# Kernel optimization log

Measured on AMD Instinct MI355X. Metric: run time of the kernel, lower is better.

## Reference

```python
import jax, jax.numpy as jnp
import numpy as np

N = 100_000   # nodes
E = 1_600_000 # edges
D = 64        # in = hidden = out channels
EPS = 1e-8


def setup_inputs() -> dict:
    key = jax.random.key(0)
    ks = jax.random.split(key, 6)
    s = 1.0 / np.sqrt(D)
    return {
        "x": jax.random.normal(ks[0], (N, D), jnp.float32),
        "edge_index": jax.random.randint(ks[1], (2, E), 0, N, dtype=jnp.int32),
        "W0": jax.random.normal(ks[2], (D, D), jnp.float32) * s,
        "b0": jnp.zeros((D,), jnp.float32),
        "Wm": jax.random.normal(ks[3], (D, D), jnp.float32) * s,
        "bm": jnp.zeros((D,), jnp.float32),
        "W1": jax.random.normal(ks[4], (D, D), jnp.float32) * s,
        "b1": jnp.zeros((D,), jnp.float32),
    }


def _proj_normalize(y):
    # projective (hyperbolic) renormalization onto the unit sphere in R^D
    return y / (jnp.linalg.norm(y, axis=-1, keepdims=True) + EPS)


def _hyp_linear(x, W, b):
    return _proj_normalize(x @ W + b)


def _hinner(u, v):
    # UHG (hyperbolic) bilinear form: <u,v> = u_1..d-1 . v_1..d-1 - u_d * v_d
    return jnp.sum(u[..., :-1] * v[..., :-1], axis=-1) - u[..., -1] * v[..., -1]


def _cross_ratio(x):
    a, b, c, d = x[0], x[1], x[2], x[3]
    return (_hinner(a, c) * _hinner(b, d)) / (_hinner(a, d) * _hinner(b, c) + EPS)


def _maybe_restore_cr(x, cr_init):
    # restore_cross_ratio: rescale x so the 4-point cross-ratio matches cr_init,
    # applied only when the torch guard conditions hold (finite, non-degenerate).
    cr_cur = _cross_ratio(x[:4])
    ratio = cr_init / (cr_cur + EPS)
    cond = ((~jnp.isnan(cr_cur)) & (~jnp.isnan(cr_init))
            & (jnp.abs(cr_cur) > EPS) & (jnp.abs(cr_init) > EPS)
            & (ratio > EPS))
    scale = jnp.where(cond, jnp.sqrt(jnp.abs(ratio)), 1.0)
    x_r = x * scale
    ok = jnp.all(jnp.isfinite(x_r))
    return jnp.where(cond & ok, x_r, x)


def _message_passing(x, src, dst, Wm, bm):
    # gather -> mean-aggregate(scatter) -> hyperbolic linear, preserving cross-ratio
    cr0 = _cross_ratio(x[:4])
    msgs = x[src]                                                  # [E, D] gather
    summed = jax.ops.segment_sum(msgs, dst, num_segments=N)        # [N, D] scatter-add
    cnt = jax.ops.segment_sum(jnp.ones((E,), x.dtype), dst, num_segments=N)
    agg = summed / jnp.maximum(cnt, 1.0)[:, None]                  # mean aggregation
    h = _proj_normalize(agg @ Wm + bm)
    return _maybe_restore_cr(h, cr0)


def reference(x, edge_index, W0, b0, Wm, bm, W1, b1):
    src, dst = edge_index[0], edge_index[1]
    cr_init = _cross_ratio(x[:4])          # N > 3 so has_cr is always True
    h = _hyp_linear(x, W0, b0)             # layers[0]
    # num_layers = 2 -> single message-passing round (i = 1)
    h = _message_passing(h, src, dst, Wm, bm)
    h = _hyp_linear(h, W1, b1)             # layers[1]
    h = jax.nn.relu(h)                      # act
    h = _maybe_restore_cr(h, cr_init)
    return h
```

## Files before the change

kernel.cpp:

```cpp
#include <hip/hip_runtime.h>
#include <math.h>

#define NNODES 100000
#define NEDGES 1600000
#define DD 64
#define EPS 1e-8f

#define NBUCK 1024
#define BW 98
#define BIN_BLOCKS 256
#define BIN_CHUNK ((NEDGES + BIN_BLOCKS - 1) / BIN_BLOCKS)
#define BIN_CAP 12
#define CAPB 1792
#define SORT_CAP 4096
#define NTILES (NNODES / 16)
#define CAP4 512
#define TSTR 68

typedef unsigned short us8 __attribute__((ext_vector_type(8)));
typedef short short8 __attribute__((ext_vector_type(8)));
typedef float f32x4 __attribute__((ext_vector_type(4)));

__device__ __forceinline__ float wave_sum(float v) {
    #pragma unroll
    for (int off = 32; off; off >>= 1) v += __shfl_xor(v, off, 64);
    return v;
}

__device__ __forceinline__ float hinner(float u, float v, float sgn) {
    return wave_sum(sgn * u * v);
}

__device__ __forceinline__ float cross_ratio(float r0, float r1, float r2, float r3, float sgn) {
    float A = hinner(r0, r2, sgn);
    float B = hinner(r1, r3, sgn);
    float C = hinner(r0, r3, sgn);
    float Dv = hinner(r1, r2, sgn);
    return (A * B) / (C * Dv + EPS);
}

__device__ __forceinline__ float restore_scale(float cr_i, float cr_c) {
    float ratio = cr_i / (cr_c + EPS);
    bool cond = (!__builtin_isnan(cr_c)) && (!__builtin_isnan(cr_i)) &&
                (fabsf(cr_c) > EPS) && (fabsf(cr_i) > EPS) && (ratio > EPS);
    float s = 1.0f;
    if (cond) {
        s = sqrtf(fabsf(ratio));
        if (!__builtin_isfinite(s)) s = 1.0f;
    }
    return s;
}

__device__ __forceinline__ unsigned short f2bf(float f) {
    unsigned u = __float_as_uint(f);
    unsigned r = (u + 0x7fffu + ((u >> 16) & 1u)) >> 16;
    return (unsigned short)r;
}

__device__ __forceinline__ float bf2f(unsigned short b) {
    return __uint_as_float(((unsigned)b) << 16);
}

__device__ __forceinline__ float bcast(float v, int lane) {
    return __int_as_float(__builtin_amdgcn_readlane(__float_as_int(v), lane));
}

__device__ __forceinline__ void load_bfrags(const float* __restrict__ W, int lane,
                                            short8 bhi[4][2], short8 blo[4][2]) {
    int c = lane & 15, q = lane >> 4;
    #pragma unroll
    for (int t = 0; t < 4; t++)
        #pragma unroll
        for (int h = 0; h < 2; h++) {
            short8 hi8, lo8;
            #pragma unroll
            for (int j = 0; j < 8; j++) {
                float w = W[(h * 32 + q * 8 + j) * DD + t * 16 + c];
                unsigned short hb = f2bf(w);
                float r = w - bf2f(hb);
                hi8[j] = (short)hb;
                lo8[j] = (short)f2bf(r);
            }
            bhi[t][h] = hi8;
            blo[t][h] = lo8;
        }
}

__device__ __forceinline__ void build_a8(const float av[8], short8& hi, short8& lo) {
    short8 h8, l8;
    #pragma unroll
    for (int j = 0; j < 8; j++) {
        unsigned short hb = f2bf(av[j]);
        float r = av[j] - bf2f(hb);
        h8[j] = (short)hb;
        l8[j] = (short)f2bf(r);
    }
    hi = h8;
    lo = l8;
}

__device__ __forceinline__ void build_a(const float* p, short8& hi, short8& lo) {
    float4 f0 = *(const float4*)p;
    float4 f1 = *(const float4*)(p + 4);
    float av[8] = {f0.x, f0.y, f0.z, f0.w, f1.x, f1.y, f1.z, f1.w};
    build_a8(av, hi, lo);
}

__device__ __forceinline__ void store_split(unsigned short* __restrict__ aggh,
                                            int node, int q, const float* s, float inv) {
    short8 hi8, lo8;
    #pragma unroll
    for (int i = 0; i < 8; i++) {
        float v = s[i] * inv;
        unsigned short hb = f2bf(v);
        hi8[i] = (short)hb;
        lo8[i] = (short)f2bf(v - bf2f(hb));
    }
    unsigned short* p = aggh + (size_t)node * 128 + q * 16;
    *(short8*)p = hi8;
    *(short8*)(p + 8) = lo8;
}

#define MFMA3R(cacc, ahi, alo, BH, BL, t, h)                                     \
    cacc = __builtin_amdgcn_mfma_f32_16x16x32_bf16(ahi, BH[t][h], cacc, 0, 0, 0); \
    cacc = __builtin_amdgcn_mfma_f32_16x16x32_bf16(alo, BH[t][h], cacc, 0, 0, 0); \
    cacc = __builtin_amdgcn_mfma_f32_16x16x32_bf16(ahi, BL[t][h], cacc, 0, 0, 0);

__device__ __forceinline__ void l0_tiles(const float* __restrict__ x,
                                         const float* __restrict__ W0,
                                         const float* __restrict__ b0,
                                         unsigned short* __restrict__ h0b,
                                         int lane, int wid, int nw, int tlo, int thi) {
    int c = lane & 15, q = lane >> 4;
    short8 bhi[4][2], blo[4][2];
    load_bfrags(W0, lane, bhi, blo);
    float badd[4];
    #pragma unroll
    for (int t = 0; t < 4; t++) badd[t] = b0[t * 16 + c];
    for (int tile = tlo + wid; tile < thi; tile += nw) {
        int R = tile * 16;
        f32x4 cc[4] = {{0, 0, 0, 0}, {0, 0, 0, 0}, {0, 0, 0, 0}, {0, 0, 0, 0}};
        #pragma unroll
        for (int hh = 0; hh < 2; hh++) {
            short8 ahi, alo;
            build_a(x + ((size_t)(R + c) << 6) + hh * 32 + q * 8, ahi, alo);
            #pragma unroll
            for (int t = 0; t < 4; t++) { MFMA3R(cc[t], ahi, alo, bhi, blo, t, hh); }
        }
        float ss[4];
        #pragma unroll
        for (int r = 0; r < 4; r++) {
            #pragma unroll
            for (int t = 0; t < 4; t++) cc[t][r] += badd[t];
            ss[r] = cc[0][r] * cc[0][r] + cc[1][r] * cc[1][r] +
                    cc[2][r] * cc[2][r] + cc[3][r] * cc[3][r];
        }
        #pragma unroll
        for (int off = 1; off <= 8; off <<= 1) {
            #pragma unroll
            for (int r = 0; r < 4; r++) ss[r] += __shfl_xor(ss[r], off, 64);
        }
        #pragma unroll
        for (int r = 0; r < 4; r++) {
            float sc = 1.0f / (sqrtf(ss[r]) + EPS);
            int row = R + q * 4 + r;
            #pragma unroll
            for (int t = 0; t < 4; t++)
                h0b[(size_t)row * DD + t * 16 + c] = f2bf(cc[t][r] * sc);
        }
    }
}

__global__ __launch_bounds__(256, 3) void k_binGemm(const float* __restrict__ x,
                                                    const float* __restrict__ W0,
                                                    const float* __restrict__ b0,
                                                    unsigned short* __restrict__ h0b,
                                                    const int* __restrict__ ei,
                                                    int* __restrict__ cursor,
                                                    unsigned* __restrict__ colpack,
                                                    int* __restrict__ cnt4,
                                                    int* __restrict__ list4) {
    __shared__ unsigned stag[NBUCK * BIN_CAP];
    __shared__ int lcnt[NBUCK];
    int t = threadIdx.x;
    if (blockIdx.x < BIN_BLOCKS) {
        for (int i = t; i < NBUCK; i += 256) lcnt[i] = 0;
        __syncthreads();
        int lo = blockIdx.x * BIN_CHUNK;
        int hi = lo + BIN_CHUNK; if (hi > NEDGES) hi = NEDGES;
        for (int e = lo + t; e < hi; e += 256) {
            int d = ei[NEDGES + e];
            int s = ei[e];
            if ((unsigned)d < 4u) {
                int p = atomicAdd(&cnt4[d], 1);
                if (p < CAP4) list4[d * CAP4 + p] = s;
            }
            unsigned b = (unsigned)d / BW;
            unsigned dl = (unsigned)d - b * BW;
            unsigned pk = ((unsigned)s << 8) | dl;
            int slot = atomicAdd(&lcnt[b], 1);
            if (slot < BIN_CAP) {
                stag[b * BIN_CAP + slot] = pk;
            } else {
                colpack[b * CAPB + atomicAdd(&cursor[b], 1)] = pk;
            }
        }
        __syncthreads();
        for (int b = t; b < NBUCK; b += 256) {
            int cnt = lcnt[b];
            if (cnt > BIN_CAP) cnt = BIN_CAP;
            if (cnt > 0) {
                int base = b * CAPB + atomicAdd(&cursor[b], cnt);
                for (int i = 0; i < cnt; i++)
                    colpack[base + i] = stag[b * BIN_CAP + i];
            }
        }
        return;
    }
    int bid = blockIdx.x - BIN_BLOCKS;
    int wid = (bid * 256 + t) >> 6;
    l0_tiles(x, W0, b0, h0b, t & 63, wid, 4096, 0, NTILES);
}

__global__ __launch_bounds__(512, 4) void k_sortAggH(const unsigned* __restrict__ colpack,
                                                     const int* __restrict__ cursor,
                                                     const unsigned short* __restrict__ h0b,
                                                     unsigned short* __restrict__ aggh,
                                                     const float* __restrict__ x,
                                                     const float* __restrict__ W0,
                                                     const float* __restrict__ b0,
                                                     const int* __restrict__ cnt4,
                                                     const int* __restrict__ list4,
                                                     const float* __restrict__ Wm,
                                                     const float* __restrict__ bm,
                                                     const float* __restrict__ W1,
                                                     const float* __restrict__ b1,
                                                     float* __restrict__ scal) {
    __shared__ int lcol[SORT_CAP];
    __shared__ int cnt[BW];
    __shared__ int pre[BW];
    int t = threadIdx.x;
    if (blockIdx.x == 0) {
        float* hs  = (float*)lcol;
        float* h2s = hs + 4 * DD;
        float* frs = h2s + 4 * DD;
        int lane = t & 63;
        int w = t >> 6;
        float sgn = (lane == 63) ? -1.0f : 1.0f;
        float s1 = 1.0f;
        float cr_init = 0.0f;
        if (w < 4) {
            float w0[DD];
            #pragma unroll
            for (int k = 0; k < DD; k++) w0[k] = W0[k * DD + lane];
            float b0v = b0[lane];
            auto h0row = [&](int r) -> float {
                float xv = x[(size_t)r * DD + lane];
                float acc = b0v;
                #pragma unroll
                for (int k = 0; k < DD; k++)
                    acc = fmaf(bcast(xv, k), w0[k], acc);
                float n = sqrtf(wave_sum(acc * acc));
                return acc / (n + EPS);
            };
            hs[w * DD + lane] = h0row(w);
            int full = cnt4[w];
            int cl = full; if (cl > CAP4) cl = CAP4;
            float sum = 0.0f;
            for (int i = 0; i < cl; i++) sum += h0row(list4[w * CAP4 + i]);
            float av = sum / fmaxf((float)full, 1.0f);
            float acc = bm[lane];
            #pragma unroll
            for (int k = 0; k < DD; k++)
                acc = fmaf(bcast(av, k), Wm[k * DD + lane], acc);
            float n = sqrtf(wave_sum(acc * acc));
            h2s[w * DD + lane] = acc / (n + EPS);
        }
        __syncthreads();
        if (w < 4) {
            cr_init = cross_ratio(x[lane], x[DD + lane], x[2 * DD + lane], x[3 * DD + lane], sgn);
            float cr0 = cross_ratio(hs[lane], hs[DD + lane], hs[2 * DD + lane], hs[3 * DD + lane], sgn);
            float cr_cur = cross_ratio(h2s[lane], h2s[DD + lane], h2s[2 * DD + lane], h2s[3 * DD + lane], sgn);
            s1 = restore_scale(cr0, cr_cur);
            float hv = h2s[w * DD + lane] * s1;
            float acc2 = b1[lane];
            #pragma unroll
            for (int k = 0; k < DD; k++)
                acc2 = fmaf(bcast(hv, k), W1[k * DD + lane], acc2);
            float n = sqrtf(wave_sum(acc2 * acc2));
            frs[w * DD + lane] = fmaxf(acc2 / (n + EPS), 0.0f);
        }
        __syncthreads();
        if (w == 0) {
            float cr2 = cross_ratio(frs[lane], frs[DD + lane], frs[2 * DD + lane], frs[3 * DD + lane], sgn);
            float s2 = restore_scale(cr_init, cr2);
            if (lane == 0) { scal[0] = s1; scal[1] = s2; }
        }
        return;
    }
    int b = blockIdx.x - 1;
    int nlo = b * BW; if (nlo > NNODES) nlo = NNODES;
    int nhi = nlo + BW; if (nhi > NNODES) nhi = NNODES;
    int nodes = nhi - nlo;
    int base = b * CAPB;
    int n = cursor[b];
    if (n > CAPB) n = CAPB;
    for (int i = t; i < BW; i += 512) cnt[i] = 0;
    __syncthreads();
    for (int i = t; i < n; i += 512)
        atomicAdd(&cnt[colpack[base + i] & 255u], 1);
    __syncthreads();
    if (t < 64) {
        int v0 = cnt[t];
        int inc0 = v0;
        #pragma unroll
        for (int off = 1; off < 64; off <<= 1) {
            int u = __shfl_up(inc0, off, 64);
            if (t >= off) inc0 += u;
        }
        int tot0 = __builtin_amdgcn_readlane(inc0, 63);
        int ex0 = inc0 - v0;
        int i1 = 64 + t;
        int v1 = (i1 < BW) ? cnt[i1] : 0;
        int inc1 = v1;
        #pragma unroll
        for (int off = 1; off < 64; off <<= 1) {
            int u = __shfl_up(inc1, off, 64);
            if (t >= off) inc1 += u;
        }
        int ex1 = inc1 - v1 + tot0;
        pre[t] = ex0;
        cnt[t] = ex0;
        if (i1 < BW) { pre[i1] = ex1; cnt[i1] = ex1; }
    }
    __syncthreads();
    for (int i = t; i < n; i += 512) {
        unsigned pk = colpack[base + i];
        int pos = atomicAdd(&cnt[pk & 255u], 1);
        lcol[pos] = (int)(pk >> 8);
    }
    __syncthreads();
    int wv = t >> 6, lane = t & 63;
    int q = lane & 7, g = lane >> 3;
    for (int dA = wv; dA < nodes; dA += 32) {
        int dB = dA + 8, dC = dA + 16, dD = dA + 24;
        bool hB = dB < nodes, hC = dC < nodes, hD = dD < nodes;
        int stA = pre[dA], enA = cnt[dA];
        int stB = hB ? pre[dB] : 0, enB = hB ? cnt[dB] : 0;
        int stC = hC ? pre[dC] : 0, enC = hC ? cnt[dC] : 0;
        int stD = hD ? pre[dD] : 0, enD = hD ? cnt[dD] : 0;
        int ngA = (enA - stA + 7) >> 3, ngB = (enB - stB + 7) >> 3;
        int ngC = (enC - stC + 7) >> 3, ngD = (enD - stD + 7) >> 3;
        int ng = ngA > ngB ? ngA : ngB;
        if (ngC > ng) ng = ngC;
        if (ngD > ng) ng = ngD;
        float sA[8] = {0, 0, 0, 0, 0, 0, 0, 0};
        float sB[8] = {0, 0, 0, 0, 0, 0, 0, 0};
        float sC[8] = {0, 0, 0, 0, 0, 0, 0, 0};
        float sD[8] = {0, 0, 0, 0, 0, 0, 0, 0};
        for (int k = 0; k < ng; k++) {
            int eA = stA + k * 8 + g;
            int eB = stB + k * 8 + g;
            int eC = stC + k * 8 + g;
            int eD = stD + k * 8 + g;
            bool fA = eA < enA, fB = eB < enB, fC = eC < enC, fD = eD < enD;
            int iA = lcol[fA ? eA : 0];
            int iB = lcol[fB ? eB : 0];
            int iC = lcol[fC ? eC : 0];
            int iD = lcol[fD ? eD : 0];
            us8 uA = *(const us8*)(h0b + (size_t)iA * DD + q * 8);
            us8 uB = *(const us8*)(h0b + (size_t)iB * DD + q * 8);
            us8 uC = *(const us8*)(h0b + (size_t)iC * DD + q * 8);
            us8 uD = *(const us8*)(h0b + (size_t)iD * DD + q * 8);
            float mA = fA ? 1.0f : 0.0f;
            float mB = fB ? 1.0f : 0.0f;
            float mC = fC ? 1.0f : 0.0f;
            float mD = fD ? 1.0f : 0.0f;
            #pragma unroll
            for (int i = 0; i < 8; i++) {
                sA[i] = fmaf(mA, bf2f(uA[i]), sA[i]);
                sB[i] = fmaf(mB, bf2f(uB[i]), sB[i]);
                sC[i] = fmaf(mC, bf2f(uC[i]), sC[i]);
                sD[i] = fmaf(mD, bf2f(uD[i]), sD[i]);
            }
        }
        #pragma unroll
        for (int i = 0; i < 8; i++) {
            sA[i] += __shfl_xor(sA[i], 8, 64);
            sA[i] += __shfl_xor(sA[i], 16, 64);
            sA[i] += __shfl_xor(sA[i], 32, 64);
            sB[i] += __shfl_xor(sB[i], 8, 64);
            sB[i] += __shfl_xor(sB[i], 16, 64);
            sB[i] += __shfl_xor(sB[i], 32, 64);
            sC[i] += __shfl_xor(sC[i], 8, 64);
            sC[i] += __shfl_xor(sC[i], 16, 64);
            sC[i] += __shfl_xor(sC[i], 32, 64);
            sD[i] += __shfl_xor(sD[i], 8, 64);
            sD[i] += __shfl_xor(sD[i], 16, 64);
            sD[i] += __shfl_xor(sD[i], 32, 64);
        }
        if (g == 0) {
            store_split(aggh, nlo + dA, q, sA, 1.0f / fmaxf((float)(enA - stA), 1.0f));
            if (hB) store_split(aggh, nlo + dB, q, sB, 1.0f / fmaxf((float)(enB - stB), 1.0f));
            if (hC) store_split(aggh, nlo + dC, q, sC, 1.0f / fmaxf((float)(enC - stC), 1.0f));
            if (hD) store_split(aggh, nlo + dD, q, sD, 1.0f / fmaxf((float)(enD - stD), 1.0f));
        }
    }
}

__global__ __launch_bounds__(256, 2) void k_gemm2(unsigned short* __restrict__ dataH,
                                                  float* __restrict__ outp,
                                                  const float* __restrict__ Wm,
                                                  const float* __restrict__ bm,
                                                  const float* __restrict__ W1,
                                                  const float* __restrict__ b1,
                                                  const float* __restrict__ scal) {
    __shared__ float tsm[4][16 * TSTR];
    int tid = threadIdx.x;
    int wv = tid >> 6, lane = tid & 63;
    int c = lane & 15, q = lane >> 4;
    short8 bhiM[4][2], bloM[4][2], bhi1[4][2], blo1[4][2];
    load_bfrags(Wm, lane, bhiM, bloM);
    load_bfrags(W1, lane, bhi1, blo1);
    float bmv[4], b1v[4];
    #pragma unroll
    for (int t = 0; t < 4; t++) { bmv[t] = bm[t * 16 + c]; b1v[t] = b1[t * 16 + c]; }
    float s1 = scal[0], s2 = scal[1];
    int wid = (blockIdx.x * 256 + tid) >> 6;
    int nw = (gridDim.x * 256) >> 6;
    for (int tile = wid; tile < NTILES; tile += nw) {
        int R = tile * 16;
        f32x4 cc[4] = {{0, 0, 0, 0}, {0, 0, 0, 0}, {0, 0, 0, 0}, {0, 0, 0, 0}};
        #pragma unroll
        for (int hh = 0; hh < 2; hh++) {
            const unsigned short* p = dataH + (size_t)(R + c) * 128 + (hh * 4 + q) * 16;
            short8 ahi = *(const short8*)p;
            short8 alo = *(const short8*)(p + 8);
            #pragma unroll
            for (int t = 0; t < 4; t++) { MFMA3R(cc[t], ahi, alo, bhiM, bloM, t, hh); }
        }
        float ss[4];
        #pragma unroll
        for (int r = 0; r < 4; r++) {
            #pragma unroll
            for (int t = 0; t < 4; t++) cc[t][r] += bmv[t];
            ss[r] = cc[0][r] * cc[0][r] + cc[1][r] * cc[1][r] +
                    cc[2][r] * cc[2][r] + cc[3][r] * cc[3][r];
        }
        #pragma unroll
        for (int off = 1; off <= 8; off <<= 1) {
            #pragma unroll
            for (int r = 0; r < 4; r++) ss[r] += __shfl_xor(ss[r], off, 64);
        }
        #pragma unroll
        for (int r = 0; r < 4; r++) {
            float sc = s1 / (sqrtf(ss[r]) + EPS);
            #pragma unroll
            for (int t = 0; t < 4; t++)
                tsm[wv][(q * 4 + r) * TSTR + t * 16 + c] = cc[t][r] * sc;
        }
        f32x4 c2[4] = {{0, 0, 0, 0}, {0, 0, 0, 0}, {0, 0, 0, 0}, {0, 0, 0, 0}};
        #pragma unroll
        for (int hh = 0; hh < 2; hh++) {
            const float* p = &tsm[wv][c * TSTR + hh * 32 + q * 8];
            float av[8];
            #pragma unroll
            for (int j = 0; j < 8; j++) av[j] = p[j];
            short8 ahi, alo;
            build_a8(av, ahi, alo);
            #pragma unroll
            for (int t = 0; t < 4; t++) { MFMA3R(c2[t], ahi, alo, bhi1, blo1, t, hh); }
        }
        #pragma unroll
        for (int r = 0; r < 4; r++) {
            #pragma unroll
            for (int t = 0; t < 4; t++) c2[t][r] += b1v[t];
            ss[r] = c2[0][r] * c2[0][r] + c2[1][r] * c2[1][r] +
                    c2[2][r] * c2[2][r] + c2[3][r] * c2[3][r];
        }
        #pragma unroll
        for (int off = 1; off <= 8; off <<= 1) {
            #pragma unroll
            for (int r = 0; r < 4; r++) ss[r] += __shfl_xor(ss[r], off, 64);
        }
        #pragma unroll
        for (int r = 0; r < 4; r++) {
            float sc = 1.0f / (sqrtf(ss[r]) + EPS);
            int row = R + q * 4 + r;
            #pragma unroll
            for (int t = 0; t < 4; t++)
                outp[(size_t)row * DD + t * 16 + c] = fmaxf(c2[t][r] * sc, 0.0f) * s2;
        }
    }
}

extern "C" void kernel_launch(void* const* d_in, const int* in_sizes, int n_in,
                              void* d_out, int out_size, void* d_ws, size_t ws_size,
                              hipStream_t stream) {
    const float* x  = (const float*)d_in[0];
    const int*   ei = (const int*)d_in[1];
    const float* W0 = (const float*)d_in[2];
    const float* b0 = (const float*)d_in[3];
    const float* Wm = (const float*)d_in[4];
    const float* bm = (const float*)d_in[5];
    const float* W1 = (const float*)d_in[6];
    const float* b1 = (const float*)d_in[7];
    float* out = (float*)d_out;
    unsigned short* outH = (unsigned short*)d_out;

    unsigned short* h0b = (unsigned short*)d_ws;
    unsigned* colpack = (unsigned*)(h0b + (size_t)NNODES * DD);
    int* cursor = (int*)(colpack + (size_t)NBUCK * CAPB);
    int* cnt4   = cursor + NBUCK;
    int* list4  = cnt4 + 4;
    float* scal = (float*)(list4 + 4 * CAP4);

    (void)hipMemsetAsync(cursor, 0, (NBUCK + 4) * sizeof(int), stream);

    k_binGemm <<<BIN_BLOCKS + 1024, 256, 0, stream>>>(x, W0, b0, h0b, ei, cursor,
                                                      colpack, cnt4, list4);
    k_sortAggH<<<NBUCK, 512, 0, stream>>>(colpack, cursor, h0b, outH,
                                          x, W0, b0, cnt4, list4, Wm, bm, W1, b1, scal);
    k_gemm2   <<<512, 256, 0, stream>>>(outH, out, Wm, bm, W1, b1, scal);
}
```

Before: 185.2 us.

## Fuse Wm hyperbolic linear into aggregation kernel via LDS staging

The aggregation kernel now stages each bucket's mean-aggregated rows as split bf16 hi/lo in shared memory, then runs the Wm GEMM plus row normalization in-block and writes the normalized result to global. The final kernel only does the W1 GEMM, folding the s1 restore scale algebraically into the accumulator (s1*acc + b1), and launches with more blocks. This removes the intermediate shared-memory round trip and the second GEMM from the last kernel, at the cost of more LDS per aggregation block (a staging buffer), a zeroing pass, and scalar 2-byte global stores that may coalesce poorly.

```diff
diff --git a/kernel.cpp b/kernel.cpp
--- a/kernel.cpp
+++ b/kernel.cpp
@@ -12,10 +12,9 @@
 #define BIN_CHUNK ((NEDGES + BIN_BLOCKS - 1) / BIN_BLOCKS)
 #define BIN_CAP 12
 #define CAPB 1792
-#define SORT_CAP 4096
 #define NTILES (NNODES / 16)
 #define CAP4 512
-#define TSTR 68
+#define SROW 136
 
 typedef unsigned short us8 __attribute__((ext_vector_type(8)));
 typedef short short8 __attribute__((ext_vector_type(8)));
@@ -104,21 +103,6 @@
     float4 f1 = *(const float4*)(p + 4);
     float av[8] = {f0.x, f0.y, f0.z, f0.w, f1.x, f1.y, f1.z, f1.w};
     build_a8(av, hi, lo);
-}
-
-__device__ __forceinline__ void store_split(unsigned short* __restrict__ aggh,
-                                            int node, int q, const float* s, float inv) {
-    short8 hi8, lo8;
-    #pragma unroll
-    for (int i = 0; i < 8; i++) {
-        float v = s[i] * inv;
-        unsigned short hb = f2bf(v);
-        hi8[i] = (short)hb;
-        lo8[i] = (short)f2bf(v - bf2f(hb));
-    }
-    unsigned short* p = aggh + (size_t)node * 128 + q * 16;
-    *(short8*)p = hi8;
-    *(short8*)(p + 8) = lo8;
 }
 
 #define MFMA3R(cacc, ahi, alo, BH, BL, t, h)                                     \
@@ -236,12 +220,13 @@
                                                      const float* __restrict__ W1,
                                                      const float* __restrict__ b1,
                                                      float* __restrict__ scal) {
-    __shared__ int lcol[SORT_CAP];
+    __shared__ int lcol[CAPB];
     __shared__ int cnt[BW];
     __shared__ int pre[BW];
+    __shared__ unsigned short stage[112 * SROW];
     int t = threadIdx.x;
     if (blockIdx.x == 0) {
-        float* hs  = (float*)lcol;
+        float* hs  = (float*)stage;
         float* h2s = hs + 4 * DD;
         float* frs = h2s + 4 * DD;
         int lane = t & 63;
@@ -306,6 +291,10 @@
     int n = cursor[b];
     if (n > CAPB) n = CAPB;
     for (int i = t; i < BW; i += 512) cnt[i] = 0;
+    {
+        int* sz = (int*)stage;
+        for (int i = t; i < (112 * SROW) / 2; i += 512) sz[i] = 0;
+    }
     __syncthreads();
     for (int i = t; i < n; i += 512)
         atomicAdd(&cnt[colpack[base + i] & 255u], 1);
@@ -400,31 +389,96 @@
             sD[i] += __shfl_xor(sD[i], 32, 64);
         }
         if (g == 0) {
-            store_split(aggh, nlo + dA, q, sA, 1.0f / fmaxf((float)(enA - stA), 1.0f));
-            if (hB) store_split(aggh, nlo + dB, q, sB, 1.0f / fmaxf((float)(enB - stB), 1.0f));
-            if (hC) store_split(aggh, nlo + dC, q, sC, 1.0f / fmaxf((float)(enC - stC), 1.0f));
-            if (hD) store_split(aggh, nlo + dD, q, sD, 1.0f / fmaxf((float)(enD - stD), 1.0f));
-        }
-    }
-}
-
-__global__ __launch_bounds__(256, 2) void k_gemm2(unsigned short* __restrict__ dataH,
+            float invs[4] = {1.0f / fmaxf((float)(enA - stA), 1.0f),
+                             1.0f / fmaxf((float)(enB - stB), 1.0f),
+                             1.0f / fmaxf((float)(enC - stC), 1.0f),
+                             1.0f / fmaxf((float)(enD - stD), 1.0f)};
+            const float* sp[4] = {sA, sB, sC, sD};
+            int dls[4] = {dA, dB, dC, dD};
+            bool hv[4] = {true, hB, hC, hD};
+            #pragma unroll
+            for (int u = 0; u < 4; u++) {
+                if (!hv[u]) continue;
+                short8 hi8, lo8;
+                #pragma unroll
+                for (int i = 0; i < 8; i++) {
+                    float v = sp[u][i] * invs[u];
+                    unsigned short hb = f2bf(v);
+                    hi8[i] = (short)hb;
+                    lo8[i] = (short)f2bf(v - bf2f(hb));
+                }
+                unsigned short* p = stage + dls[u] * SROW + q * 16;
+                *(short8*)p = hi8;
+                *(short8*)(p + 8) = lo8;
+            }
+        }
+    }
+    __syncthreads();
+    int ntile = (nodes + 15) >> 4;
+    if (wv < ntile) {
+        int c16 = lane & 15, q4 = lane >> 4;
+        short8 bhiM[4][2], bloM[4][2];
+        load_bfrags(Wm, lane, bhiM, bloM);
+        float bmv[4];
+        #pragma unroll
+        for (int tt = 0; tt < 4; tt++) bmv[tt] = bm[tt * 16 + c16];
+        int Rl = wv * 16;
+        f32x4 cm[4] = {{0, 0, 0, 0}, {0, 0, 0, 0}, {0, 0, 0, 0}, {0, 0, 0, 0}};
+        #pragma unroll
+        for (int hh = 0; hh < 2; hh++) {
+            const unsigned short* p = stage + (Rl + c16) * SROW + (hh * 4 + q4) * 16;
+            short8 ahi = *(const short8*)p;
+            short8 alo = *(const short8*)(p + 8);
+            #pragma unroll
+            for (int tt = 0; tt < 4; tt++) { MFMA3R(cm[tt], ahi, alo, bhiM, bloM, tt, hh); }
+        }
+        float ss[4];
+        #pragma unroll
+        for (int r = 0; r < 4; r++) {
+            #pragma unroll
+            for (int tt = 0; tt < 4; tt++) cm[tt][r] += bmv[tt];
+            ss[r] = cm[0][r] * cm[0][r] + cm[1][r] * cm[1][r] +
+                    cm[2][r] * cm[2][r] + cm[3][r] * cm[3][r];
+        }
+        #pragma unroll
+        for (int off = 1; off <= 8; off <<= 1) {
+            #pragma unroll
+            for (int r = 0; r < 4; r++) ss[r] += __shfl_xor(ss[r], off, 64);
+        }
+        #pragma unroll
+        for (int r = 0; r < 4; r++) {
+            float sc = 1.0f / (sqrtf(ss[r]) + EPS);
+            int row = Rl + q4 * 4 + r;
+            if (row < nodes) {
+                size_t gb = (size_t)(nlo + row) * 128;
+                int ch = (c16 >> 3);
+                int el = c16 & 7;
+                #pragma unroll
+                for (int tt = 0; tt < 4; tt++) {
+                    float v = cm[tt][r] * sc;
+                    unsigned short hb = f2bf(v);
+                    unsigned short lb = f2bf(v - bf2f(hb));
+                    aggh[gb + (2 * tt + ch) * 16 + el] = hb;
+                    aggh[gb + (2 * tt + ch) * 16 + 8 + el] = lb;
+                }
+            }
+        }
+    }
+}
+
+__global__ __launch_bounds__(256, 4) void k_gemm1(const unsigned short* __restrict__ dataH,
                                                   float* __restrict__ outp,
-                                                  const float* __restrict__ Wm,
-                                                  const float* __restrict__ bm,
                                                   const float* __restrict__ W1,
                                                   const float* __restrict__ b1,
                                                   const float* __restrict__ scal) {
-    __shared__ float tsm[4][16 * TSTR];
     int tid = threadIdx.x;
-    int wv = tid >> 6, lane = tid & 63;
+    int lane = tid & 63;
     int c = lane & 15, q = lane >> 4;
-    short8 bhiM[4][2], bloM[4][2], bhi1[4][2], blo1[4][2];
-    load_bfrags(Wm, lane, bhiM, bloM);
-    load_bfrags(W1, lane, bhi1, blo1);
-    float bmv[4], b1v[4];
+    short8 bhi[4][2], blo[4][2];
+    load_bfrags(W1, lane, bhi, blo);
+    float badd[4];
     #pragma unroll
-    for (int t = 0; t < 4; t++) { bmv[t] = bm[t * 16 + c]; b1v[t] = b1[t * 16 + c]; }
+    for (int t = 0; t < 4; t++) badd[t] = b1[t * 16 + c];
     float s1 = scal[0], s2 = scal[1];
     int wid = (blockIdx.x * 256 + tid) >> 6;
     int nw = (gridDim.x * 256) >> 6;
@@ -437,46 +491,15 @@
             short8 ahi = *(const short8*)p;
             short8 alo = *(const short8*)(p + 8);
             #pragma unroll
-            for (int t = 0; t < 4; t++) { MFMA3R(cc[t], ahi, alo, bhiM, bloM, t, hh); }
+            for (int t = 0; t < 4; t++) { MFMA3R(cc[t], ahi, alo, bhi, blo, t, hh); }
         }
         float ss[4];
         #pragma unroll
         for (int r = 0; r < 4; r++) {
             #pragma unroll
-            for (int t = 0; t < 4; t++) cc[t][r] += bmv[t];
+            for (int t = 0; t < 4; t++) cc[t][r] = s1 * cc[t][r] + badd[t];
             ss[r] = cc[0][r] * cc[0][r] + cc[1][r] * cc[1][r] +
                     cc[2][r] * cc[2][r] + cc[3][r] * cc[3][r];
-        }
-        #pragma unroll
-        for (int off = 1; off <= 8; off <<= 1) {
-            #pragma unroll
-            for (int r = 0; r < 4; r++) ss[r] += __shfl_xor(ss[r], off, 64);
-        }
-        #pragma unroll
-        for (int r = 0; r < 4; r++) {
-            float sc = s1 / (sqrtf(ss[r]) + EPS);
-            #pragma unroll
-            for (int t = 0; t < 4; t++)
-                tsm[wv][(q * 4 + r) * TSTR + t * 16 + c] = cc[t][r] * sc;
-        }
-        f32x4 c2[4] = {{0, 0, 0, 0}, {0, 0, 0, 0}, {0, 0, 0, 0}, {0, 0, 0, 0}};
-        #pragma unroll
-        for (int hh = 0; hh < 2; hh++) {
-            const float* p = &tsm[wv][c * TSTR + hh * 32 + q * 8];
-            float av[8];
-            #pragma unroll
-            for (int j = 0; j < 8; j++) av[j] = p[j];
-            short8 ahi, alo;
-            build_a8(av, ahi, alo);
-            #pragma unroll
-            for (int t = 0; t < 4; t++) { MFMA3R(c2[t], ahi, alo, bhi1, blo1, t, hh); }
-        }
-        #pragma unroll
-        for (int r = 0; r < 4; r++) {
-            #pragma unroll
-            for (int t = 0; t < 4; t++) c2[t][r] += b1v[t];
-            ss[r] = c2[0][r] * c2[0][r] + c2[1][r] * c2[1][r] +
-                    c2[2][r] * c2[2][r] + c2[3][r] * c2[3][r];
         }
         #pragma unroll
         for (int off = 1; off <= 8; off <<= 1) {
@@ -489,7 +512,7 @@
             int row = R + q * 4 + r;
             #pragma unroll
             for (int t = 0; t < 4; t++)
-                outp[(size_t)row * DD + t * 16 + c] = fmaxf(c2[t][r] * sc, 0.0f) * s2;
+                outp[(size_t)row * DD + t * 16 + c] = fmaxf(cc[t][r] * sc, 0.0f) * s2;
         }
     }
 }
@@ -521,5 +544,5 @@
                                                       colpack, cnt4, list4);
     k_sortAggH<<<NBUCK, 512, 0, stream>>>(colpack, cursor, h0b, outH,
                                           x, W0, b0, cnt4, list4, Wm, bm, W1, b1, scal);
-    k_gemm2   <<<512, 256, 0, stream>>>(outH, out, Wm, bm, W1, b1, scal);
-}
+    k_gemm1   <<<1024, 256, 0, stream>>>(outH, out, W1, b1, scal);
+}
```

After: 196.3 us. +6.0%, slower.
